# Performance work log

Hardware: AMD Instinct MI355X
Metric: run time of the kernel (lower is better)

Reference implementation:

```python
import jax, jax.numpy as jnp
import numpy as np

N, F, T, C, E = 5000, 4, 12, 600, 160000


def setup_inputs() -> dict:
    key = jax.random.key(0)
    ks = jax.random.split(key, 18)
    x = jax.random.normal(ks[0], (N, F, T), jnp.float32)
    edge_index = jax.random.randint(ks[1], (2, E), 0, N)
    edge_attributes = jax.random.uniform(ks[2], (E,), jnp.float32)
    s_in = 0.5   # glorot-ish scale for F->C conv weights
    s_lin = 0.03  # scale for (2C)->C gate linears
    return {
        "x": x,
        "edge_index": edge_index,
        "edge_attributes": edge_attributes,
        # GCNConv weights/biases for z, r, h gates (weight stored [F, C])
        "W_z": jax.random.normal(ks[3], (F, C), jnp.float32) * s_in,
        "b_z": jnp.zeros((C,), jnp.float32),
        "W_r": jax.random.normal(ks[4], (F, C), jnp.float32) * s_in,
        "b_r": jnp.zeros((C,), jnp.float32),
        "W_h": jax.random.normal(ks[5], (F, C), jnp.float32) * s_in,
        "b_h": jnp.zeros((C,), jnp.float32),
        # gate Linear(2C, C) weights in torch layout [out=C, in=2C]
        "Wlz": jax.random.normal(ks[6], (C, 2 * C), jnp.float32) * s_lin,
        "blz": jnp.zeros((C,), jnp.float32),
        "Wlr": jax.random.normal(ks[7], (C, 2 * C), jnp.float32) * s_lin,
        "blr": jnp.zeros((C,), jnp.float32),
        "Wlh": jax.random.normal(ks[8], (C, 2 * C), jnp.float32) * s_lin,
        "blh": jnp.zeros((C,), jnp.float32),
        # temporal attention logits over periods
        "att": jax.random.normal(ks[9], (T,), jnp.float32),
        # head Linear(600, periods), torch layout [T, C]
        "W_head": jax.random.normal(ks[10], (T, C), jnp.float32) * 0.04,
        "b_head": jnp.zeros((T,), jnp.float32),
    }


def _gcn_propagate(x, edge_index, edge_weight):
    """A_hat @ x with A_hat = D^{-1/2}(A+I)D^{-1/2} (GCNConv norm, self-loops w=1).
    x: [N, F, T] -> [N, F, T]."""
    loop = jnp.arange(N)
    row = jnp.concatenate([edge_index[0], loop])   # source j
    col = jnp.concatenate([edge_index[1], loop])   # target i
    w = jnp.concatenate([edge_weight, jnp.ones((N,), x.dtype)])
    deg = jax.ops.segment_sum(w, col, num_segments=N)
    dis = jnp.where(deg > 0, jax.lax.rsqrt(deg), 0.0)
    norm = dis[row] * w * dis[col]                 # [E+N]
    msgs = norm[:, None, None] * x[row]            # gather + scale, [E+N, F, T]
    return jax.ops.segment_sum(msgs, col, num_segments=N)


def reference(x, edge_index, edge_attributes,
              W_z, b_z, W_r, b_r, W_h, b_h,
              Wlz, blz, Wlr, blr, Wlh, blh,
              att, W_head, b_head):
    # A3TGCN: H is passed as None each period -> zeros, never threaded across
    # time. Hence z*H == 0 and the H*r candidate term == 0 exactly; the r-gate
    # (W_r, b_r, Wlr, blr) and the second halves of Wlz/Wlh drop out of the math.
    agg = _gcn_propagate(x, edge_index, edge_attributes)          # [N, F, T]
    # GCNConv output = A_hat X W + b (linear commutes with propagation)
    conv_z = jnp.einsum('nft,fc->nct', agg, W_z) + b_z[:, None]   # [N, C, T]
    conv_h = jnp.einsum('nft,fc->nct', agg, W_h) + b_h[:, None]
    # gate linears on cat([conv, H]) with H = 0 -> only first C input columns
    z = jax.nn.sigmoid(jnp.einsum('nct,dc->ndt', conv_z, Wlz[:, :C]) + blz[:, None])
    h_tilde = jnp.tanh(jnp.einsum('nct,dc->ndt', conv_h, Wlh[:, :C]) + blh[:, None])
    H_t = (1.0 - z) * h_tilde                                      # z*H = 0
    probs = jax.nn.softmax(att)                                    # [T]
    H_accum = jnp.einsum('nct,t->nc', H_t, probs)                  # [N, C]
    return jax.nn.relu(H_accum) @ W_head.T + b_head                # [N, T]
```

## Files before the change

### kernel.cpp

```cpp
#include <hip/hip_runtime.h>

#define NN 5000
#define NF 4
#define NT 12
#define NC 600
#define NE 160000
#define FT 48
#define LOG2E 1.4426950408889634f

typedef float v2f __attribute__((ext_vector_type(2)));


__global__ void k_init(int* __restrict__ cnt) {
    int i = blockIdx.x * blockDim.x + threadIdx.x;
    if (i < NN) cnt[i] = 0;
}

__global__ void k_count(const int* __restrict__ ei, int* __restrict__ cnt,
                        int* __restrict__ rank) {
    int e = blockIdx.x * blockDim.x + threadIdx.x;
    if (e < NE) rank[e] = atomicAdd(&cnt[ei[NE + e]], 1);
}

#define SCAN_CHUNK 20
__global__ __launch_bounds__(256) void k_scan(const int* __restrict__ cnt,
                                              int* __restrict__ base) {
    __shared__ int part[256];
    int t = threadIdx.x;
    int start = t * SCAN_CHUNK;
    int s = 0;
#pragma unroll
    for (int k = 0; k < SCAN_CHUNK; ++k) {
        int idx = start + k;
        if (idx < NN) s += cnt[idx];
    }
    part[t] = s;
    __syncthreads();
    for (int off = 1; off < 256; off <<= 1) {
        int v = (t >= off) ? part[t - off] : 0;
        __syncthreads();
        part[t] += v;
        __syncthreads();
    }
    int running = (t == 0) ? 0 : part[t - 1];
#pragma unroll
    for (int k = 0; k < SCAN_CHUNK; ++k) {
        int idx = start + k;
        if (idx < NN) {
            base[idx] = running;
            running += cnt[idx];
        }
    }
    if (t == 255) base[NN] = part[255];
}

__global__ void k_scatter(const int* __restrict__ ei, const float* __restrict__ w,
                          const int* __restrict__ base, const int* __restrict__ rank,
                          int2* __restrict__ epak) {
    int e = blockIdx.x * blockDim.x + threadIdx.x;
    if (e < NE) {
        int2 p; p.x = ei[e]; p.y = __float_as_int(w[e]);
        epak[base[ei[NE + e]] + rank[e]] = p;
    }
}

__global__ __launch_bounds__(64) void k_deg_dis(const int2* __restrict__ epak,
                                                const int* __restrict__ base,
                                                float* __restrict__ dis) {
    int n = blockIdx.x;
    int lane = threadIdx.x;
    int b0 = base[n], b1 = base[n + 1];
    float s = 0.f;
    for (int j = b0 + lane; j < b1; j += 64) s += __int_as_float(epak[j].y);
#pragma unroll
    for (int off = 32; off > 0; off >>= 1) s += __shfl_down(s, off, 64);
    if (lane == 0) dis[n] = rsqrtf(1.0f + s);
}

__global__ __launch_bounds__(64) void k_gather(
        const float* __restrict__ x, const float* __restrict__ dis,
        const int2* __restrict__ epak, const int* __restrict__ base,
        float* __restrict__ agg) {
    int n = blockIdx.x;
    int lane = threadIdx.x;
    int b0 = base[n], b1 = base[n + 1];
    float dn = dis[n];
    float acc = 0.f;
    if (lane < FT) acc = dn * x[n * FT + lane];
    int j = b0;
    for (; j + 3 < b1; j += 4) {
        int2 p0 = epak[j], p1 = epak[j + 1], p2 = epak[j + 2], p3 = epak[j + 3];
        float n0 = dis[p0.x] * __int_as_float(p0.y);
        float n1 = dis[p1.x] * __int_as_float(p1.y);
        float n2 = dis[p2.x] * __int_as_float(p2.y);
        float n3 = dis[p3.x] * __int_as_float(p3.y);
        if (lane < FT) {
            acc += n0 * x[p0.x * FT + lane];
            acc += n1 * x[p1.x * FT + lane];
            acc += n2 * x[p2.x * FT + lane];
            acc += n3 * x[p3.x * FT + lane];
        }
    }
    for (; j < b1; ++j) {
        int2 p0 = epak[j];
        float n0 = dis[p0.x] * __int_as_float(p0.y);
        if (lane < FT) acc += n0 * x[p0.x * FT + lane];
    }
    if (lane < FT) agg[n * FT + lane] = dn * acc;
}

__global__ __launch_bounds__(256) void k_weights(
        const float* __restrict__ Wz, const float* __restrict__ bz,
        const float* __restrict__ Wh, const float* __restrict__ bh,
        const float* __restrict__ Wlz, const float* __restrict__ blz,
        const float* __restrict__ Wlh, const float* __restrict__ blh,
        const float* __restrict__ att,
        float* __restrict__ Mz4, float* __restrict__ Mh4,
        float* __restrict__ bzh, float* __restrict__ probs) {
    int wid = blockIdx.x * 4 + (threadIdx.x >> 6);
    int lane = threadIdx.x & 63;
    if (wid >= 6012) return;

    if (wid < 6000) {
        const float* va;
        const float* vb;
        float scale, bias = 0.f;
        if (wid < 2400) {
            int f = wid / NC, d = wid % NC;
            va = Wz + f * NC; vb = Wlz + d * (2 * NC); scale = LOG2E;
        } else if (wid < 4800) {
            int j = wid - 2400;
            int f = j / NC, d = j % NC;
            va = Wh + f * NC; vb = Wlh + d * (2 * NC); scale = 2.0f * LOG2E;
        } else if (wid < 5400) {
            int d = wid - 4800;
            va = bz; vb = Wlz + d * (2 * NC); scale = LOG2E; bias = blz[d];
        } else {
            int d = wid - 5400;
            va = bh; vb = Wlh + d * (2 * NC); scale = 2.0f * LOG2E; bias = blh[d];
        }
        float s = 0.f;
        for (int c = lane; c < NC; c += 64) s = fmaf(va[c], vb[c], s);
#pragma unroll
        for (int off = 32; off > 0; off >>= 1) s += __shfl_down(s, off, 64);
        if (lane == 0) {
            float r = scale * (bias + s);
            if (wid < 2400) {
                int f = wid / NC, d = wid % NC;
                Mz4[d * 4 + f] = r;
            } else if (wid < 4800) {
                int j = wid - 2400;
                int f = j / NC, d = j % NC;
                Mh4[d * 4 + f] = r;
            } else if (wid < 5400) {
                bzh[(wid - 4800) * 2] = r;
            } else {
                bzh[(wid - 5400) * 2 + 1] = r;
            }
        }
    } else if (lane == 0) {
        int t = wid - 6000;
        float m = att[0];
        for (int k = 1; k < NT; ++k) m = fmaxf(m, att[k]);
        float ssum = 0.f;
        for (int k = 0; k < NT; ++k) ssum += __expf(att[k] - m);
        probs[t] = __expf(att[t] - m) / ssum;
    }
}

__global__ void k_wt(const float* __restrict__ Whead, float* __restrict__ WT) {
    int i = blockIdx.x * blockDim.x + threadIdx.x;
    if (i < NC * NT) WT[i] = Whead[(i % NT) * NC + (i / NT)];
}

__global__ __launch_bounds__(256, 4) void k_main(
        const float* __restrict__ agg,
        const float4* __restrict__ Mz4, const float4* __restrict__ Mh4,
        const float2* __restrict__ bzh, const float* __restrict__ probs,
        const float* __restrict__ WT, const float* __restrict__ bhead,
        float* __restrict__ out) {
    int wid = threadIdx.x >> 6, lane = threadIdx.x & 63;
    int n = blockIdx.x * 4 + wid;

    const v2f* ag2 = (const v2f*)(agg + n * FT);
    v2f A2[24];
#pragma unroll
    for (int i = 0; i < 24; ++i) A2[i] = ag2[i];

    v2f pp[6];
#pragma unroll
    for (int tp = 0; tp < 6; ++tp) { pp[tp].x = probs[2 * tp]; pp[tp].y = probs[2 * tp + 1]; }

    float outp[NT];
#pragma unroll
    for (int t = 0; t < NT; ++t) outp[t] = 0.f;

#pragma unroll
    for (int it = 0; it < 10; ++it) {
        int d = it * 64 + lane;
        bool act = d < NC;
        int dd = act ? d : 0;

        float4 mzv = Mz4[dd];
        float4 mhv = Mh4[dd];
        float2 bb = bzh[dd];

        v2f hacc; hacc.x = 0.f; hacc.y = 0.f;
#pragma unroll
        for (int tp = 0; tp < 6; ++tp) {
            v2f u; u.x = bb.x; u.y = bb.x;
            v2f v; v.x = bb.y; v.y = bb.y;
            u += A2[0 * 6 + tp] * mzv.x;
            u += A2[1 * 6 + tp] * mzv.y;
            u += A2[2 * 6 + tp] * mzv.z;
            u += A2[3 * 6 + tp] * mzv.w;
            v += A2[0 * 6 + tp] * mhv.x;
            v += A2[1 * 6 + tp] * mhv.y;
            v += A2[2 * 6 + tp] * mhv.z;
            v += A2[3 * 6 + tp] * mhv.w;
            v2f eu; eu.x = exp2f(u.x); eu.y = exp2f(u.y);
            v2f ev; ev.x = exp2f(v.x); ev.y = exp2f(v.y);
            v2f den = (eu + 1.f) * (ev + 1.f);
            v2f rd; rd.x = __builtin_amdgcn_rcpf(den.x); rd.y = __builtin_amdgcn_rcpf(den.y);
            v2f num = pp[tp] * (ev - 1.f);
            hacc += num * rd;
        }
        float r = act ? fmaxf(hacc.x + hacc.y, 0.f) : 0.f;

        const float4* wt4 = (const float4*)(WT + dd * NT);
        float4 w0 = wt4[0], w1 = wt4[1], w2 = wt4[2];
        outp[0] = fmaf(r, w0.x, outp[0]);  outp[1] = fmaf(r, w0.y, outp[1]);
        outp[2] = fmaf(r, w0.z, outp[2]);  outp[3] = fmaf(r, w0.w, outp[3]);
        outp[4] = fmaf(r, w1.x, outp[4]);  outp[5] = fmaf(r, w1.y, outp[5]);
        outp[6] = fmaf(r, w1.z, outp[6]);  outp[7] = fmaf(r, w1.w, outp[7]);
        outp[8] = fmaf(r, w2.x, outp[8]);  outp[9] = fmaf(r, w2.y, outp[9]);
        outp[10] = fmaf(r, w2.z, outp[10]); outp[11] = fmaf(r, w2.w, outp[11]);
    }

    __shared__ float red[4][NT][68];
#pragma unroll
    for (int t = 0; t < NT; ++t) red[wid][t][lane] = outp[t];
    if (lane < NT) {
        const float4* row = (const float4*)red[wid][lane];
        float4 s4 = row[0];
#pragma unroll
        for (int j = 1; j < 16; ++j) {
            float4 v = row[j];
            s4.x += v.x; s4.y += v.y; s4.z += v.z; s4.w += v.w;
        }
        out[n * NT + lane] = (s4.x + s4.y) + (s4.z + s4.w) + bhead[lane];
    }
}

extern "C" void kernel_launch(void* const* d_in, const int* in_sizes, int n_in,
                              void* d_out, int out_size, void* d_ws, size_t ws_size,
                              hipStream_t stream) {
    const float* x     = (const float*)d_in[0];
    const int*   ei    = (const int*)d_in[1];
    const float* ea    = (const float*)d_in[2];
    const float* Wz    = (const float*)d_in[3];
    const float* bz    = (const float*)d_in[4];
    const float* Wh    = (const float*)d_in[7];
    const float* bh    = (const float*)d_in[8];
    const float* Wlz   = (const float*)d_in[9];
    const float* blz   = (const float*)d_in[10];
    const float* Wlh   = (const float*)d_in[13];
    const float* blh   = (const float*)d_in[14];
    const float* att   = (const float*)d_in[15];
    const float* Whead = (const float*)d_in[16];
    const float* bhead = (const float*)d_in[17];
    float* out = (float*)d_out;

    float* ws    = (float*)d_ws;
    float* dis   = ws;
    int*   cnt   = (int*)(ws + 5000);
    int*   base  = (int*)(ws + 10000);
    int*   rank  = (int*)(ws + 16000);
    int2*  epak  = (int2*)(ws + 176000);
    float* agg   = ws + 496000;
    float* Mz4   = ws + 736000;
    float* Mh4   = ws + 738400;
    float* bzh   = ws + 740800;
    float* WT    = ws + 742000;
    float* probs = ws + 749200;

    k_init<<<(NN + 255) / 256, 256, 0, stream>>>(cnt);
    k_count<<<(NE + 255) / 256, 256, 0, stream>>>(ei, cnt, rank);
    k_scan<<<1, 256, 0, stream>>>(cnt, base);
    k_scatter<<<(NE + 255) / 256, 256, 0, stream>>>(ei, ea, base, rank, epak);
    k_weights<<<(6012 + 3) / 4, 256, 0, stream>>>(Wz, bz, Wh, bh, Wlz, blz, Wlh, blh,
                                                  att, Mz4, Mh4, bzh, probs);
    k_wt<<<(NC * NT + 255) / 256, 256, 0, stream>>>(Whead, WT);
    k_deg_dis<<<NN, 64, 0, stream>>>(epak, base, dis);
    k_gather<<<NN, 64, 0, stream>>>(x, dis, epak, base, agg);
    k_main<<<NN / 4, 256, 0, stream>>>(agg, (const float4*)Mz4, (const float4*)Mh4,
                                       (const float2*)bzh, probs, WT, bhead, out);
}
```

Baseline: 79.49 us.

## Fuse degree into count, prenormalize edges, stage weight tables in LDS

The in-degree is now accumulated with float atomics during edge counting, and the inverse square root is computed in the scan kernel, which removes the separate degree kernel. The scatter kernel stores the fully normalized edge weight, so the gather no longer does a random lookup of the source node's scale per edge. The weight-transpose kernel is folded into the weight-precompute kernel, which writes one packed table. The main kernel copies that table into shared memory, processes two nodes per wavefront, and reduces with shuffles. This trades two fewer launches and cheaper loads for float-atomic contention, order-dependent summation, and lower occupancy from the large shared-memory footprint.

```diff
diff --git a/kernel.cpp b/kernel.cpp
--- a/kernel.cpp
+++ b/kernel.cpp
@@ -11,20 +11,27 @@
 typedef float v2f __attribute__((ext_vector_type(2)));
 
 
-__global__ void k_init(int* __restrict__ cnt) {
+__global__ void k_init(float* __restrict__ deg, int* __restrict__ cnt) {
     int i = blockIdx.x * blockDim.x + threadIdx.x;
-    if (i < NN) cnt[i] = 0;
-}
-
-__global__ void k_count(const int* __restrict__ ei, int* __restrict__ cnt,
+    if (i < NN) { deg[i] = 1.0f; cnt[i] = 0; }
+}
+
+__global__ void k_count(const int* __restrict__ ei, const float* __restrict__ w,
+                        int* __restrict__ cnt, float* __restrict__ deg,
                         int* __restrict__ rank) {
     int e = blockIdx.x * blockDim.x + threadIdx.x;
-    if (e < NE) rank[e] = atomicAdd(&cnt[ei[NE + e]], 1);
+    if (e < NE) {
+        int c = ei[NE + e];
+        rank[e] = atomicAdd(&cnt[c], 1);
+        atomicAdd(&deg[c], w[e]);
+    }
 }
 
 #define SCAN_CHUNK 20
 __global__ __launch_bounds__(256) void k_scan(const int* __restrict__ cnt,
-                                              int* __restrict__ base) {
+                                              const float* __restrict__ deg,
+                                              int* __restrict__ base,
+                                              float* __restrict__ dis) {
     __shared__ int part[256];
     int t = threadIdx.x;
     int start = t * SCAN_CHUNK;
@@ -49,32 +56,24 @@
         if (idx < NN) {
             base[idx] = running;
             running += cnt[idx];
+            dis[idx] = rsqrtf(deg[idx]);
         }
     }
     if (t == 255) base[NN] = part[255];
 }
 
 __global__ void k_scatter(const int* __restrict__ ei, const float* __restrict__ w,
+                          const float* __restrict__ dis,
                           const int* __restrict__ base, const int* __restrict__ rank,
                           int2* __restrict__ epak) {
     int e = blockIdx.x * blockDim.x + threadIdx.x;
     if (e < NE) {
-        int2 p; p.x = ei[e]; p.y = __float_as_int(w[e]);
-        epak[base[ei[NE + e]] + rank[e]] = p;
-    }
-}
-
-__global__ __launch_bounds__(64) void k_deg_dis(const int2* __restrict__ epak,
-                                                const int* __restrict__ base,
-                                                float* __restrict__ dis) {
-    int n = blockIdx.x;
-    int lane = threadIdx.x;
-    int b0 = base[n], b1 = base[n + 1];
-    float s = 0.f;
-    for (int j = b0 + lane; j < b1; j += 64) s += __int_as_float(epak[j].y);
-#pragma unroll
-    for (int off = 32; off > 0; off >>= 1) s += __shfl_down(s, off, 64);
-    if (lane == 0) dis[n] = rsqrtf(1.0f + s);
+        int r = ei[e];
+        int c = ei[NE + e];
+        float nu = dis[r] * w[e] * dis[c];
+        int2 p; p.x = r; p.y = __float_as_int(nu);
+        epak[base[c] + rank[e]] = p;
+    }
 }
 
 __global__ __launch_bounds__(64) void k_gather(
@@ -86,14 +85,14 @@
     int b0 = base[n], b1 = base[n + 1];
     float dn = dis[n];
     float acc = 0.f;
-    if (lane < FT) acc = dn * x[n * FT + lane];
+    if (lane < FT) acc = dn * dn * x[n * FT + lane];
     int j = b0;
     for (; j + 3 < b1; j += 4) {
         int2 p0 = epak[j], p1 = epak[j + 1], p2 = epak[j + 2], p3 = epak[j + 3];
-        float n0 = dis[p0.x] * __int_as_float(p0.y);
-        float n1 = dis[p1.x] * __int_as_float(p1.y);
-        float n2 = dis[p2.x] * __int_as_float(p2.y);
-        float n3 = dis[p3.x] * __int_as_float(p3.y);
+        float n0 = __int_as_float(p0.y);
+        float n1 = __int_as_float(p1.y);
+        float n2 = __int_as_float(p2.y);
+        float n3 = __int_as_float(p3.y);
         if (lane < FT) {
             acc += n0 * x[p0.x * FT + lane];
             acc += n1 * x[p1.x * FT + lane];
@@ -103,10 +102,10 @@
     }
     for (; j < b1; ++j) {
         int2 p0 = epak[j];
-        float n0 = dis[p0.x] * __int_as_float(p0.y);
+        float n0 = __int_as_float(p0.y);
         if (lane < FT) acc += n0 * x[p0.x * FT + lane];
     }
-    if (lane < FT) agg[n * FT + lane] = dn * acc;
+    if (lane < FT) agg[n * FT + lane] = acc;
 }
 
 __global__ __launch_bounds__(256) void k_weights(
@@ -114,12 +113,11 @@
         const float* __restrict__ Wh, const float* __restrict__ bh,
         const float* __restrict__ Wlz, const float* __restrict__ blz,
         const float* __restrict__ Wlh, const float* __restrict__ blh,
-        const float* __restrict__ att,
-        float* __restrict__ Mz4, float* __restrict__ Mh4,
-        float* __restrict__ bzh, float* __restrict__ probs) {
+        const float* __restrict__ att, const float* __restrict__ Whead,
+        float* __restrict__ tabG) {
     int wid = blockIdx.x * 4 + (threadIdx.x >> 6);
     int lane = threadIdx.x & 63;
-    if (wid >= 6012) return;
+    if (wid >= 6125) return;
 
     if (wid < 6000) {
         const float* va;
@@ -147,108 +145,128 @@
             float r = scale * (bias + s);
             if (wid < 2400) {
                 int f = wid / NC, d = wid % NC;
-                Mz4[d * 4 + f] = r;
+                tabG[d * 4 + f] = r;
             } else if (wid < 4800) {
                 int j = wid - 2400;
                 int f = j / NC, d = j % NC;
-                Mh4[d * 4 + f] = r;
+                tabG[2400 + d * 4 + f] = r;
             } else if (wid < 5400) {
-                bzh[(wid - 4800) * 2] = r;
+                tabG[4800 + (wid - 4800) * 2] = r;
             } else {
-                bzh[(wid - 5400) * 2 + 1] = r;
+                tabG[4800 + (wid - 5400) * 2 + 1] = r;
             }
         }
-    } else if (lane == 0) {
-        int t = wid - 6000;
-        float m = att[0];
-        for (int k = 1; k < NT; ++k) m = fmaxf(m, att[k]);
-        float ssum = 0.f;
-        for (int k = 0; k < NT; ++k) ssum += __expf(att[k] - m);
-        probs[t] = __expf(att[t] - m) / ssum;
-    }
-}
-
-__global__ void k_wt(const float* __restrict__ Whead, float* __restrict__ WT) {
-    int i = blockIdx.x * blockDim.x + threadIdx.x;
-    if (i < NC * NT) WT[i] = Whead[(i % NT) * NC + (i / NT)];
-}
-
-__global__ __launch_bounds__(256, 4) void k_main(
-        const float* __restrict__ agg,
-        const float4* __restrict__ Mz4, const float4* __restrict__ Mh4,
-        const float2* __restrict__ bzh, const float* __restrict__ probs,
-        const float* __restrict__ WT, const float* __restrict__ bhead,
-        float* __restrict__ out) {
-    int wid = threadIdx.x >> 6, lane = threadIdx.x & 63;
-    int n = blockIdx.x * 4 + wid;
-
-    const v2f* ag2 = (const v2f*)(agg + n * FT);
-    v2f A2[24];
-#pragma unroll
-    for (int i = 0; i < 24; ++i) A2[i] = ag2[i];
-
+    } else if (wid < 6012) {
+        if (lane == 0) {
+            int t = wid - 6000;
+            float m = att[0];
+            for (int k = 1; k < NT; ++k) m = fmaxf(m, att[k]);
+            float ssum = 0.f;
+            for (int k = 0; k < NT; ++k) ssum += __expf(att[k] - m);
+            tabG[13200 + t] = __expf(att[t] - m) / ssum;
+        }
+    } else {
+        int i = (wid - 6012) * 64 + lane;
+        if (i < 7200) {
+            int j = i & 3;
+            int rest = i >> 2;
+            int d = rest % NC, q = rest / NC;
+            tabG[6000 + i] = Whead[(4 * q + j) * NC + d];
+        }
+    }
+}
+
+__global__ __launch_bounds__(256, 2) void k_main(
+        const float* __restrict__ agg, const float* __restrict__ tabG,
+        const float* __restrict__ bhead, float* __restrict__ out) {
+    __shared__ float tab[13212];
+    __shared__ float red[4][NT][16];
+    int tid = threadIdx.x;
+
+    {
+        const float4* s4 = (const float4*)tabG;
+        float4* d4 = (float4*)tab;
+        for (int i = tid; i < 3303; i += 256) d4[i] = s4[i];
+    }
+    __syncthreads();
+
+    int wid = tid >> 6, lane = tid & 63;
+    const float4* mz4 = (const float4*)tab;
+    const float4* mh4 = (const float4*)(tab + 2400);
+    const float2* bzh = (const float2*)(tab + 4800);
+    const float4* wt4 = (const float4*)(tab + 6000);
     v2f pp[6];
 #pragma unroll
-    for (int tp = 0; tp < 6; ++tp) { pp[tp].x = probs[2 * tp]; pp[tp].y = probs[2 * tp + 1]; }
-
-    float outp[NT];
-#pragma unroll
-    for (int t = 0; t < NT; ++t) outp[t] = 0.f;
-
-#pragma unroll
-    for (int it = 0; it < 10; ++it) {
-        int d = it * 64 + lane;
-        bool act = d < NC;
-        int dd = act ? d : 0;
-
-        float4 mzv = Mz4[dd];
-        float4 mhv = Mh4[dd];
-        float2 bb = bzh[dd];
-
-        v2f hacc; hacc.x = 0.f; hacc.y = 0.f;
-#pragma unroll
-        for (int tp = 0; tp < 6; ++tp) {
-            v2f u; u.x = bb.x; u.y = bb.x;
-            v2f v; v.x = bb.y; v.y = bb.y;
-            u += A2[0 * 6 + tp] * mzv.x;
-            u += A2[1 * 6 + tp] * mzv.y;
-            u += A2[2 * 6 + tp] * mzv.z;
-            u += A2[3 * 6 + tp] * mzv.w;
-            v += A2[0 * 6 + tp] * mhv.x;
-            v += A2[1 * 6 + tp] * mhv.y;
-            v += A2[2 * 6 + tp] * mhv.z;
-            v += A2[3 * 6 + tp] * mhv.w;
-            v2f eu; eu.x = exp2f(u.x); eu.y = exp2f(u.y);
-            v2f ev; ev.x = exp2f(v.x); ev.y = exp2f(v.y);
-            v2f den = (eu + 1.f) * (ev + 1.f);
-            v2f rd; rd.x = __builtin_amdgcn_rcpf(den.x); rd.y = __builtin_amdgcn_rcpf(den.y);
-            v2f num = pp[tp] * (ev - 1.f);
-            hacc += num * rd;
-        }
-        float r = act ? fmaxf(hacc.x + hacc.y, 0.f) : 0.f;
-
-        const float4* wt4 = (const float4*)(WT + dd * NT);
-        float4 w0 = wt4[0], w1 = wt4[1], w2 = wt4[2];
-        outp[0] = fmaf(r, w0.x, outp[0]);  outp[1] = fmaf(r, w0.y, outp[1]);
-        outp[2] = fmaf(r, w0.z, outp[2]);  outp[3] = fmaf(r, w0.w, outp[3]);
-        outp[4] = fmaf(r, w1.x, outp[4]);  outp[5] = fmaf(r, w1.y, outp[5]);
-        outp[6] = fmaf(r, w1.z, outp[6]);  outp[7] = fmaf(r, w1.w, outp[7]);
-        outp[8] = fmaf(r, w2.x, outp[8]);  outp[9] = fmaf(r, w2.y, outp[9]);
-        outp[10] = fmaf(r, w2.z, outp[10]); outp[11] = fmaf(r, w2.w, outp[11]);
-    }
-
-    __shared__ float red[4][NT][68];
-#pragma unroll
-    for (int t = 0; t < NT; ++t) red[wid][t][lane] = outp[t];
-    if (lane < NT) {
-        const float4* row = (const float4*)red[wid][lane];
-        float4 s4 = row[0];
-#pragma unroll
-        for (int j = 1; j < 16; ++j) {
-            float4 v = row[j];
-            s4.x += v.x; s4.y += v.y; s4.z += v.z; s4.w += v.w;
-        }
-        out[n * NT + lane] = (s4.x + s4.y) + (s4.z + s4.w) + bhead[lane];
+    for (int tp = 0; tp < 6; ++tp) { pp[tp].x = tab[13200 + 2 * tp]; pp[tp].y = tab[13200 + 2 * tp + 1]; }
+
+#pragma unroll
+    for (int half = 0; half < 2; ++half) {
+        int n = blockIdx.x * 8 + wid * 2 + half;
+
+        const v2f* ag2 = (const v2f*)(agg + n * FT);
+        v2f A2[24];
+#pragma unroll
+        for (int i = 0; i < 24; ++i) A2[i] = ag2[i];
+
+        float outp[NT];
+#pragma unroll
+        for (int t = 0; t < NT; ++t) outp[t] = 0.f;
+
+#pragma unroll
+        for (int it = 0; it < 10; ++it) {
+            int d = it * 64 + lane;
+            bool act = d < NC;
+            int dd = act ? d : 0;
+
+            float4 mzv = mz4[dd];
+            float4 mhv = mh4[dd];
+            float2 bb = bzh[dd];
+
+            v2f hacc; hacc.x = 0.f; hacc.y = 0.f;
+#pragma unroll
+            for (int tp = 0; tp < 6; ++tp) {
+                v2f u; u.x = bb.x; u.y = bb.x;
+                v2f v; v.x = bb.y; v.y = bb.y;
+                u += A2[0 * 6 + tp] * mzv.x;
+                u += A2[1 * 6 + tp] * mzv.y;
+                u += A2[2 * 6 + tp] * mzv.z;
+                u += A2[3 * 6 + tp] * mzv.w;
+                v += A2[0 * 6 + tp] * mhv.x;
+                v += A2[1 * 6 + tp] * mhv.y;
+                v += A2[2 * 6 + tp] * mhv.z;
+                v += A2[3 * 6 + tp] * mhv.w;
+                v2f eu; eu.x = exp2f(u.x); eu.y = exp2f(u.y);
+                v2f ev; ev.x = exp2f(v.x); ev.y = exp2f(v.y);
+                v2f den = (eu + 1.f) * (ev + 1.f);
+                v2f rd; rd.x = __builtin_amdgcn_rcpf(den.x); rd.y = __builtin_amdgcn_rcpf(den.y);
+                v2f num = pp[tp] * (ev - 1.f);
+                hacc += num * rd;
+            }
+            float r = act ? fmaxf(hacc.x + hacc.y, 0.f) : 0.f;
+
+            float4 w0 = wt4[0 * NC + dd], w1 = wt4[1 * NC + dd], w2 = wt4[2 * NC + dd];
+            outp[0]  = fmaf(r, w0.x, outp[0]);   outp[1]  = fmaf(r, w0.y, outp[1]);
+            outp[2]  = fmaf(r, w0.z, outp[2]);   outp[3]  = fmaf(r, w0.w, outp[3]);
+            outp[4]  = fmaf(r, w1.x, outp[4]);   outp[5]  = fmaf(r, w1.y, outp[5]);
+            outp[6]  = fmaf(r, w1.z, outp[6]);   outp[7]  = fmaf(r, w1.w, outp[7]);
+            outp[8]  = fmaf(r, w2.x, outp[8]);   outp[9]  = fmaf(r, w2.y, outp[9]);
+            outp[10] = fmaf(r, w2.z, outp[10]);  outp[11] = fmaf(r, w2.w, outp[11]);
+        }
+
+#pragma unroll
+        for (int t = 0; t < NT; ++t) {
+            float v = outp[t];
+            v += __shfl_xor(v, 32, 64);
+            v += __shfl_xor(v, 16, 64);
+            if (lane < 16) red[wid][t][lane] = v;
+        }
+        if (lane < NT) {
+            const float4* row = (const float4*)red[wid][lane];
+            float4 a = row[0], b = row[1], c = row[2], d = row[3];
+            float s = ((a.x + a.y) + (a.z + a.w)) + ((b.x + b.y) + (b.z + b.w))
+                    + ((c.x + c.y) + (c.z + c.w)) + ((d.x + d.y) + (d.z + d.w));
+            out[n * NT + lane] = s + bhead[lane];
+        }
     }
 }
 
@@ -271,28 +289,22 @@
     const float* bhead = (const float*)d_in[17];
     float* out = (float*)d_out;
 
-    float* ws    = (float*)d_ws;
-    float* dis   = ws;
-    int*   cnt   = (int*)(ws + 5000);
-    int*   base  = (int*)(ws + 10000);
-    int*   rank  = (int*)(ws + 16000);
-    int2*  epak  = (int2*)(ws + 176000);
-    float* agg   = ws + 496000;
-    float* Mz4   = ws + 736000;
-    float* Mh4   = ws + 738400;
-    float* bzh   = ws + 740800;
-    float* WT    = ws + 742000;
-    float* probs = ws + 749200;
-
-    k_init<<<(NN + 255) / 256, 256, 0, stream>>>(cnt);
-    k_count<<<(NE + 255) / 256, 256, 0, stream>>>(ei, cnt, rank);
-    k_scan<<<1, 256, 0, stream>>>(cnt, base);
-    k_scatter<<<(NE + 255) / 256, 256, 0, stream>>>(ei, ea, base, rank, epak);
-    k_weights<<<(6012 + 3) / 4, 256, 0, stream>>>(Wz, bz, Wh, bh, Wlz, blz, Wlh, blh,
-                                                  att, Mz4, Mh4, bzh, probs);
-    k_wt<<<(NC * NT + 255) / 256, 256, 0, stream>>>(Whead, WT);
-    k_deg_dis<<<NN, 64, 0, stream>>>(epak, base, dis);
+    float* ws   = (float*)d_ws;
+    float* deg  = ws;
+    float* dis  = ws + 5000;
+    int*   cnt  = (int*)(ws + 10000);
+    int*   base = (int*)(ws + 15000);
+    int*   rank = (int*)(ws + 20008);
+    int2*  epak = (int2*)(ws + 180008);
+    float* agg  = ws + 500008;
+    float* tabG = ws + 740008;
+
+    k_init<<<(NN + 255) / 256, 256, 0, stream>>>(deg, cnt);
+    k_count<<<(NE + 255) / 256, 256, 0, stream>>>(ei, ea, cnt, deg, rank);
+    k_scan<<<1, 256, 0, stream>>>(cnt, deg, base, dis);
+    k_scatter<<<(NE + 255) / 256, 256, 0, stream>>>(ei, ea, dis, base, rank, epak);
+    k_weights<<<(6125 + 3) / 4, 256, 0, stream>>>(Wz, bz, Wh, bh, Wlz, blz, Wlh, blh,
+                                                  att, Whead, tabG);
     k_gather<<<NN, 64, 0, stream>>>(x, dis, epak, base, agg);
-    k_main<<<NN / 4, 256, 0, stream>>>(agg, (const float4*)Mz4, (const float4*)Mh4,
-                                       (const float2*)bzh, probs, WT, bhead, out);
-}
+    k_main<<<NN / 8, 256, 0, stream>>>(agg, tabG, bhead, out);
+}
```

After: 101.9 us. 1.28x slower.
